# Kernel tuning notes

Measured on AMD Instinct MI355X. Metric: run time of the kernel, lower is better.

Reference implementation:

```python
import jax, jax.numpy as jnp
import numpy as np

B, N, D = 16, 8192, 64
M, S = 256, 32          # npoints, nsample
OUT = 128
RADIUS = 0.4
WC = 64                 # WeightNet output channels
BN_EPS = 1e-5
_BN_SCALE = 1.0 / np.sqrt(1.0 + BN_EPS)  # eval-mode BN, running mean 0 / var 1


def _bn(x, gamma, beta):
    shp = [1] * x.ndim
    shp[1] = -1
    return gamma.reshape(shp) * (x * _BN_SCALE) + beta.reshape(shp)


def _pdist2(a, b):
    # a (B,P,3), b (B,Q,3) -> (B,P,Q) squared distances
    return (jnp.sum(a * a, -1)[:, :, None] + jnp.sum(b * b, -1)[:, None, :]
            - 2.0 * jnp.einsum('bpd,bqd->bpq', a, b))


def _fps(xyz, npoints):
    # furthest point sampling, pointnet2 semantics (start at index 0)
    Bq, Nq, _ = xyz.shape
    first = jnp.zeros((Bq,), jnp.int32)

    def step(carry, _):
        dist, last = carry
        pt = xyz[jnp.arange(Bq), last]                   # (B,3)
        d = jnp.sum((xyz - pt[:, None, :]) ** 2, -1)
        dist = jnp.minimum(dist, d)
        nxt = jnp.argmax(dist, -1).astype(jnp.int32)
        return (dist, nxt), nxt

    init = (jnp.full((Bq, Nq), 1e10, xyz.dtype), first)
    _, rest = jax.lax.scan(step, init, None, length=npoints - 1)
    return jnp.concatenate([first[None], rest], 0).T     # (B, npoints)


def _ball_query(xyz, new_xyz, radius, nsample):
    # first `nsample` indices within radius, pad by repeating first valid index
    d2 = _pdist2(new_xyz, xyz)                           # (B,M,N)
    n = xyz.shape[1]
    key = jnp.where(d2 <= radius * radius, n - jnp.arange(n, dtype=jnp.int32), 0)
    vals, idx = jax.lax.top_k(key, nsample)              # lowest in-radius indices first
    return jnp.where(vals > 0, idx, idx[:, :, :1])


def _group(x_ch, idx):
    # x_ch (B,C,N), idx (B,M,S) -> (B,C,M,S)
    return jax.vmap(lambda f, i: f[:, i])(x_ch, idx)


def setup_inputs():
    key = jax.random.key(0)
    ks = jax.random.split(key, 8)
    f = jnp.float32

    def w(k, o, i):
        return (jax.random.normal(k, (o, i), f) / np.sqrt(i)).astype(f)

    return {
        'xyz': jax.random.uniform(ks[0], (B, N, 3), f),
        'feature': jax.random.normal(ks[1], (B, D, N), f),
        'w0': w(ks[2], WC, 3), 'b0': jnp.zeros((WC,), f), 'gamma0': jnp.ones((WC,), f), 'beta0': jnp.zeros((WC,), f),
        'w1': w(ks[3], WC, WC), 'b1': jnp.zeros((WC,), f), 'gamma1': jnp.ones((WC,), f), 'beta1': jnp.zeros((WC,), f),
        'w2': w(ks[4], WC, WC), 'b2': jnp.zeros((WC,), f),
        'wl': w(ks[5], OUT, D * WC), 'bl': jnp.zeros((OUT,), f), 'gammal': jnp.ones((OUT,), f), 'betal': jnp.zeros((OUT,), f),
        'wf': w(ks[6], OUT, D + OUT), 'bf': jnp.zeros((OUT,), f), 'gammaf': jnp.ones((OUT,), f), 'betaf': jnp.zeros((OUT,), f),
    }


def reference(xyz, feature, w0, b0, gamma0, beta0, w1, b1, gamma1, beta1, w2, b2,
              wl, bl, gammal, betal, wf, bf, gammaf, betaf):
    relu = jax.nn.relu
    # ---- furthest point sampling ----
    fidx = _fps(xyz, M)                                  # (B,M)
    new_xyz = xyz[jnp.arange(B)[:, None], fidx]          # (B,M,3)
    # ---- ball query + grouping ----
    gidx = _ball_query(xyz, new_xyz, RADIUS, S)          # (B,M,S)
    xyz_ch = jnp.transpose(xyz, (0, 2, 1))               # (B,3,N)
    grouped_xyz = _group(xyz_ch, gidx) - jnp.transpose(new_xyz, (0, 2, 1))[:, :, :, None]  # (B,3,M,S) centered
    grouped_feat = _group(feature, gidx)                 # (B,D,M,S)
    # ---- WeightNet (1x1 convs on offsets) ----
    h = relu(_bn(jnp.einsum('oc,bcms->boms', w0, grouped_xyz) + b0[None, :, None, None], gamma0, beta0))
    h = relu(_bn(jnp.einsum('oc,bcms->boms', w1, h) + b1[None, :, None, None], gamma1, beta1))
    weights = jnp.einsum('oc,bcms->boms', w2, h) + b2[None, :, None, None]  # (B,WC,M,S)
    # ---- weighted aggregation: (B,M,D,S) @ (B,M,S,WC) -> (B,M,D*WC) ----
    agg = jnp.einsum('bdms,bwms->bmdw', grouped_feat, weights).reshape(B, M, D * WC)
    new_feature = relu(_bn(jnp.einsum('od,bmd->bom', wl, agg) + bl[None, :, None], gammal, betal))  # (B,OUT,M)
    # ---- three-NN interpolation back to N points ----
    d2 = _pdist2(xyz, new_xyz)                           # (B,N,M)
    negd, nidx = jax.lax.top_k(-d2, 3)                   # 3 nearest sampled centers
    rd = 1.0 / (-negd + 1e-8)                            # reverse density on squared distance
    wts = rd / jnp.sum(rd, -1, keepdims=True)            # (B,N,3)
    gathered = jax.vmap(lambda f2, i: f2[:, i])(new_feature, nidx)  # (B,OUT,N,3)
    interp = jnp.einsum('bcnk,bnk->bcn', gathered, wts)  # (B,OUT,N)
    # ---- concat skip + final 1x1 conv ----
    cat = jnp.concatenate([interp, feature], 1)          # (B,OUT+D,N)
    return relu(_bn(jnp.einsum('oc,bcn->bon', wf, cat) + bf[None, :, None], gammaf, betaf))
```

## Files before the change

kernel.cpp:

```cpp
#include <hip/hip_runtime.h>
#include <hip/hip_bf16.h>
#include <cstdint>
#include <cstddef>

#define BB   16
#define NN   8192
#define DD   64
#define MM   256
#define SS   32
#define OUTC 128
#define WCC  64

using short8 = __attribute__((ext_vector_type(8))) short;
using f32x4  = __attribute__((ext_vector_type(4))) float;

__device__ __forceinline__ float bnf(float x, float g, float be){
    const float BNS = 0.99999500003749969f;
    return g * (x * BNS) + be;
}
__device__ __forceinline__ unsigned short f2bf(float f){
    __hip_bfloat16 h = __float2bfloat16(f);
    return *reinterpret_cast<unsigned short*>(&h);
}
__device__ __forceinline__ float bf2f(unsigned short u){
    return __uint_as_float(((unsigned)u) << 16);
}

#define PRE_GRID (16 + 2048 + 512 + 24)

__global__ __launch_bounds__(256, 1) void k_pre(const float* __restrict__ xyz, float* __restrict__ nxyz,
    const float* __restrict__ feature, unsigned short* __restrict__ featB,
    const float* __restrict__ wl, unsigned short* __restrict__ wlB,
    const float* __restrict__ wf, unsigned short* __restrict__ wfB){
  __shared__ union {
    struct {
      float sxyz[NN*3];
      float snew[MM*3];
      unsigned long long skey[2][4];
    } f;
    float tile[64][65];
  } sm;
  const int t = threadIdx.x;
  int blk = blockIdx.x;

  if (blk < 16){
    const int b = blk;
    const float* xb = xyz + (size_t)b*NN*3;
    for (int i = t; i < NN*3; i += 256) sm.f.sxyz[i] = xb[i];
    float px[32], py[32], pz[32], pn[32], dist[32];
#pragma unroll
    for (int i=0;i<32;i++){
      const int id = i*256 + t;
      px[i] = xb[id*3+0]; py[i] = xb[id*3+1]; pz[i] = xb[id*3+2];
      pn[i] = px[i]*px[i] + py[i]*py[i] + pz[i]*pz[i];
      dist[i] = 1e10f;
    }
    __syncthreads();
    float lx = sm.f.sxyz[0], ly = sm.f.sxyz[1], lz = sm.f.sxyz[2];
    if (t==0){ sm.f.snew[0]=lx; sm.f.snew[1]=ly; sm.f.snew[2]=lz; }
    for (int step=1; step<MM; ++step){
      const float nlx = -2.0f*lx, nly = -2.0f*ly, nlz = -2.0f*lz;
      const float l2s = lx*lx + ly*ly + lz*lz;
      float bv = 0.0f; int bil = 0;
#pragma unroll
      for (int i=0;i<32;i++){
        float c  = pn[i] + l2s;
        float d  = __builtin_fmaf(px[i], nlx, __builtin_fmaf(py[i], nly, __builtin_fmaf(pz[i], nlz, c)));
        float nd = fminf(dist[i], d);
        dist[i] = nd;
        bool gt = nd > bv;
        bv  = gt ? nd : bv;
        bil = gt ? i  : bil;
      }
      const int bi = bil*256 + t;
      float v = bv; int s_;
      s_ = __builtin_amdgcn_update_dpp(__float_as_int(v), __float_as_int(v), 0x111, 0xF, 0xF, 0); v = fmaxf(v, __int_as_float(s_));
      s_ = __builtin_amdgcn_update_dpp(__float_as_int(v), __float_as_int(v), 0x112, 0xF, 0xF, 0); v = fmaxf(v, __int_as_float(s_));
      s_ = __builtin_amdgcn_update_dpp(__float_as_int(v), __float_as_int(v), 0x114, 0xF, 0xF, 0); v = fmaxf(v, __int_as_float(s_));
      s_ = __builtin_amdgcn_update_dpp(__float_as_int(v), __float_as_int(v), 0x118, 0xF, 0xF, 0); v = fmaxf(v, __int_as_float(s_));
      s_ = __builtin_amdgcn_update_dpp(__float_as_int(v), __float_as_int(v), 0x142, 0xF, 0xF, 0); v = fmaxf(v, __int_as_float(s_));
      s_ = __builtin_amdgcn_update_dpp(__float_as_int(v), __float_as_int(v), 0x143, 0xF, 0xF, 0); v = fmaxf(v, __int_as_float(s_));
      const float wmax = __int_as_float(__builtin_amdgcn_readlane(__float_as_int(v), 63));
      unsigned cm = (bv == wmax) ? (unsigned)bi : 0xFFFFFFFFu;
      unsigned u_;
      u_ = (unsigned)__builtin_amdgcn_update_dpp((int)cm, (int)cm, 0x111, 0xF, 0xF, 0); cm = cm < u_ ? cm : u_;
      u_ = (unsigned)__builtin_amdgcn_update_dpp((int)cm, (int)cm, 0x112, 0xF, 0xF, 0); cm = cm < u_ ? cm : u_;
      u_ = (unsigned)__builtin_amdgcn_update_dpp((int)cm, (int)cm, 0x114, 0xF, 0xF, 0); cm = cm < u_ ? cm : u_;
      u_ = (unsigned)__builtin_amdgcn_update_dpp((int)cm, (int)cm, 0x118, 0xF, 0xF, 0); cm = cm < u_ ? cm : u_;
      u_ = (unsigned)__builtin_amdgcn_update_dpp((int)cm, (int)cm, 0x142, 0xF, 0xF, 0); cm = cm < u_ ? cm : u_;
      u_ = (unsigned)__builtin_amdgcn_update_dpp((int)cm, (int)cm, 0x143, 0xF, 0xF, 0); cm = cm < u_ ? cm : u_;
      const unsigned widx = (unsigned)__builtin_amdgcn_readlane((int)cm, 63);
      const unsigned long long key = ((unsigned long long)__float_as_uint(wmax) << 32) | (unsigned)(NN-1 - widx);

      const int p = step & 1;
      if ((t & 63) == 0) sm.f.skey[p][t>>6] = key;
      __syncthreads();
      unsigned long long k0=sm.f.skey[p][0], k1=sm.f.skey[p][1], k2=sm.f.skey[p][2], k3=sm.f.skey[p][3];
      unsigned long long ka = k0>k1?k0:k1, kb = k2>k3?k2:k3;
      unsigned long long kw = ka>kb?ka:kb;
      const int bid = (NN-1) - (int)(unsigned)(kw & 0xFFFFFFFFull);
      lx = sm.f.sxyz[bid*3+0]; ly = sm.f.sxyz[bid*3+1]; lz = sm.f.sxyz[bid*3+2];
      if (t==0){ sm.f.snew[step*3+0]=lx; sm.f.snew[step*3+1]=ly; sm.f.snew[step*3+2]=lz; }
    }
    __syncthreads();
    for (int i = t; i < MM*3; i += 256) nxyz[(size_t)b*MM*3 + i] = sm.f.snew[i];
    return;
  }
  blk -= 16;
  if (blk < 2048){
    const int b  = blk >> 7;
    const int n0 = (blk & 127) << 6;
    {
      const int d = t >> 2, j0 = (t & 3) << 4;
      const float* src = feature + ((size_t)b*DD + d)*NN + n0 + j0;
#pragma unroll
      for (int i=0;i<16;i+=4){
        float4 v = *(const float4*)(src + i);
        sm.tile[d][j0+i+0]=v.x; sm.tile[d][j0+i+1]=v.y; sm.tile[d][j0+i+2]=v.z; sm.tile[d][j0+i+3]=v.w;
      }
    }
    __syncthreads();
    {
      const int j = t >> 2, d0 = (t & 3) << 4;
      unsigned short hv[16];
#pragma unroll
      for (int i=0;i<16;i++) hv[i] = f2bf(sm.tile[d0+i][j]);
      unsigned short* dst = featB + ((size_t)b*NN + n0 + j)*64 + d0;
      *(uint4*)(dst)     = *(uint4*)(&hv[0]);
      *(uint4*)(dst + 8) = *(uint4*)(&hv[8]);
    }
    return;
  }
  blk -= 2048;
  if (blk < 512){
    int idx = (blk*256 + t)*4;
    float4 v = *(const float4*)(wl + idx);
    ushort4 h = make_ushort4(f2bf(v.x), f2bf(v.y), f2bf(v.z), f2bf(v.w));
    *(ushort4*)(wlB + idx) = h;
    return;
  }
  blk -= 512;
  {
    int idx = (blk*256 + t)*4;
    if (idx < 128*192){
      float4 v = *(const float4*)(wf + idx);
      ushort4 h = make_ushort4(f2bf(v.x), f2bf(v.y), f2bf(v.z), f2bf(v.w));
      *(ushort4*)(wfB + idx) = h;
    }
  }
}

__global__ __launch_bounds__(64) void k_bq_mlp(const float* __restrict__ xyz,
    const float* __restrict__ nxyz,
    const float* __restrict__ w0, const float* __restrict__ b0,
    const float* __restrict__ g0, const float* __restrict__ be0,
    const float* __restrict__ w1, const float* __restrict__ b1,
    const float* __restrict__ g1, const float* __restrict__ be1,
    const float* __restrict__ w2, const float* __restrict__ b2,
    int* __restrict__ gidx, float* __restrict__ wbuf){
  const int bm = blockIdx.x;
  const int b  = bm >> 8;
  const int c  = threadIdx.x;
  __shared__ int   sidx[SS];
  __shared__ float sgx[3][SS];
  __shared__ float sh0[SS][WCC];
  __shared__ float sh1[SS][WCC];

  const float w0r0 = w0[c*3+0], w0r1 = w0[c*3+1], w0r2 = w0[c*3+2];
  const float b0c=b0[c], g0c=g0[c], be0c=be0[c];
  const float b1c=b1[c], g1c=g1[c], be1c=be1[c], b2c=b2[c];
  float w1r[64], w2r[64];
#pragma unroll
  for (int i=0;i<16;i++){
    float4 v = *(const float4*)(w1 + c*64 + i*4);
    w1r[i*4+0]=v.x; w1r[i*4+1]=v.y; w1r[i*4+2]=v.z; w1r[i*4+3]=v.w;
    float4 u = *(const float4*)(w2 + c*64 + i*4);
    w2r[i*4+0]=u.x; w2r[i*4+1]=u.y; w2r[i*4+2]=u.z; w2r[i*4+3]=u.w;
  }
  const float cx = nxyz[bm*3+0], cy = nxyz[bm*3+1], cz = nxyz[bm*3+2];
  const float* xb = xyz + (size_t)b*NN*3;
  const float R2 = (float)(0.4*0.4);
  int cnt = 0;
  for (int n0=0; n0<NN && cnt<SS; n0+=64){
    int n = n0 + c;
    float dx = xb[n*3+0]-cx, dy = xb[n*3+1]-cy, dz = xb[n*3+2]-cz;
    float d2 = dx*dx+dy*dy+dz*dz;
    bool in = (d2 <= R2);
    unsigned long long mk = __ballot(in);
    int rank = cnt + (int)__popcll(mk & ((1ull<<c)-1ull));
    if (in && rank < SS) sidx[rank] = n;
    cnt += (int)__popcll(mk);
  }
  int total = min(cnt, SS);
  __syncthreads();
  int i0 = sidx[0];
  if (c >= total && c < SS) sidx[c] = i0;
  __syncthreads();
  if (c < SS){
    int p = sidx[c];
    gidx[bm*SS + c] = p;
    sgx[0][c] = xb[p*3+0]-cx;
    sgx[1][c] = xb[p*3+1]-cy;
    sgx[2][c] = xb[p*3+2]-cz;
  }
  __syncthreads();
  for (int s=0;s<SS;s++){
    float pre = w0r0*sgx[0][s] + w0r1*sgx[1][s] + w0r2*sgx[2][s] + b0c;
    sh0[s][c] = fmaxf(bnf(pre, g0c, be0c), 0.f);
  }
  __syncthreads();
  for (int s=0;s<SS;s++){
    float a = b1c;
#pragma unroll
    for (int k=0;k<64;k+=4){
      float4 h = *(const float4*)(&sh0[s][k]);
      a += w1r[k]*h.x + w1r[k+1]*h.y + w1r[k+2]*h.z + w1r[k+3]*h.w;
    }
    sh1[s][c] = fmaxf(bnf(a, g1c, be1c), 0.f);
  }
  __syncthreads();
  float* wb = wbuf + (size_t)bm*SS*WCC;
  for (int s=0;s<SS;s++){
    float a = b2c;
#pragma unroll
    for (int k=0;k<64;k+=4){
      float4 h = *(const float4*)(&sh1[s][k]);
      a += w2r[k]*h.x + w2r[k+1]*h.y + w2r[k+2]*h.z + w2r[k+3]*h.w;
    }
    wb[s*WCC + c] = a;
  }
}

__global__ __launch_bounds__(256) void k_agg(const unsigned short* __restrict__ featB,
                                             const float* __restrict__ wbuf,
                                             const int* __restrict__ gidx,
                                             unsigned short* __restrict__ aggB){
  const int bm = blockIdx.x;
  const int b  = bm >> 8;
  __shared__ float wt[SS][WCC];
  __shared__ int   sidx[SS];
  const int t = threadIdx.x;
  const float* wsrc = wbuf + (size_t)bm*SS*WCC;
#pragma unroll
  for (int i=0;i<8;i++){
    int li = t + i*256;
    ((float*)wt)[li] = wsrc[li];
  }
  if (t < SS) sidx[t] = gidx[bm*SS + t];
  __syncthreads();
  const int d  = t & 63;
  const int wg = t >> 6;
  float acc[16];
#pragma unroll
  for (int j=0;j<16;j++) acc[j]=0.f;
  const unsigned short* fb = featB + (size_t)b*NN*64;
  for (int s=0;s<SS;s++){
    float fv = bf2f(fb[(size_t)sidx[s]*64 + d]);
#pragma unroll
    for (int j=0;j<16;j++) acc[j] += fv * wt[s][wg*16+j];
  }
  unsigned short h[16];
#pragma unroll
  for (int j=0;j<16;j++) h[j] = f2bf(acc[j]);
  unsigned short* ab = aggB + (size_t)bm*4096 + d*64 + wg*16;
  *(uint4*)(ab)     = *(uint4*)(&h[0]);
  *(uint4*)(ab + 8) = *(uint4*)(&h[8]);
}

__global__ __launch_bounds__(256) void k_nf_part(const unsigned short* __restrict__ aggB,
                                                 const unsigned short* __restrict__ wlB,
                                                 float* __restrict__ part){
  const int blk = blockIdx.x;
  const int rb  = blk >> 2;
  const int ks  = blk & 3;
  const int wid = threadIdx.x >> 6, lane = threadIdx.x & 63;
  const int m0 = rb*64 + wid*16;
  const int r  = lane & 15, kg = lane >> 4;
  f32x4 acc[8];
#pragma unroll
  for (int i=0;i<8;i++) acc[i] = (f32x4){0.f,0.f,0.f,0.f};
  const short* arow = (const short*)aggB + (size_t)(m0 + r)*4096 + ks*1024 + kg*8;
  const short* brow = (const short*)wlB  + (size_t)r*4096        + ks*1024 + kg*8;
#pragma unroll 4
  for (int kc=0; kc<32; kc++){
    short8 a = *(const short8*)(arow + kc*32);
#pragma unroll
    for (int ot=0; ot<8; ot++){
      short8 bfr = *(const short8*)(brow + (size_t)ot*16*4096 + kc*32);
      acc[ot] = __builtin_amdgcn_mfma_f32_16x16x32_bf16(a, bfr, acc[ot], 0, 0, 0);
    }
  }
  float* pb = part + ((size_t)ks << 19);
#pragma unroll
  for (int ot=0; ot<8; ot++){
#pragma unroll
    for (int rr=0; rr<4; rr++){
      int row = m0 + kg*4 + rr;
      pb[(size_t)row*128 + ot*16 + r] = acc[ot][rr];
    }
  }
}

__global__ __launch_bounds__(256) void k_nf_ep(const float* __restrict__ part,
    const float* __restrict__ bl, const float* __restrict__ gl, const float* __restrict__ bel,
    float* __restrict__ nfT){
  const int gid = blockIdx.x*256 + threadIdx.x;
  const int base = gid*4;
  const int o0 = base & 127;
  float4 s0 = *(const float4*)(part + base);
  float4 s1 = *(const float4*)(part + (1<<19) + base);
  float4 s2 = *(const float4*)(part + (2<<19) + base);
  float4 s3 = *(const float4*)(part + (3<<19) + base);
  float sum[4] = {s0.x+s1.x+s2.x+s3.x, s0.y+s1.y+s2.y+s3.y,
                  s0.z+s1.z+s2.z+s3.z, s0.w+s1.w+s2.w+s3.w};
  float ov[4];
#pragma unroll
  for (int j=0;j<4;j++){
    const int o = o0 + j;
    ov[j] = fmaxf(bnf(sum[j] + bl[o], gl[o], bel[o]), 0.f);
  }
  *(float4*)(nfT + base) = make_float4(ov[0],ov[1],ov[2],ov[3]);
}

__global__ __launch_bounds__(256) void k_final(const float* __restrict__ xyz,
    const float* __restrict__ nxyz, const float* __restrict__ nfT,
    const unsigned short* __restrict__ featB, const unsigned short* __restrict__ wfB,
    const float* __restrict__ bf, const float* __restrict__ gf, const float* __restrict__ bef,
    float* __restrict__ out){
  const int blk = blockIdx.x;
  const int b  = blk >> 6;
  const int n0 = (blk & 63) << 7;
  __shared__ float snew[MM*3];
  __shared__ float sw[128][3];
  __shared__ int   si[128][3];
  const int t = threadIdx.x;
  if (t < 192){
    float4 v = *(const float4*)(nxyz + (size_t)b*MM*3 + t*4);
    snew[t*4+0]=v.x; snew[t*4+1]=v.y; snew[t*4+2]=v.z; snew[t*4+3]=v.w;
  }
  __syncthreads();
  if (t < 128){
    const int n = n0 + t;
    const float x = xyz[((size_t)b*NN+n)*3+0];
    const float y = xyz[((size_t)b*NN+n)*3+1];
    const float z = xyz[((size_t)b*NN+n)*3+2];
    float d1=1e30f, d2=1e30f, d3=1e30f; int i1=0,i2=0,i3=0;
    for (int m=0;m<MM;m++){
      float dx=x-snew[m*3+0], dy=y-snew[m*3+1], dz=z-snew[m*3+2];
      float d = dx*dx+dy*dy+dz*dz;
      if (d < d3){
        if (d < d1){ d3=d2;i3=i2; d2=d1;i2=i1; d1=d;i1=m; }
        else if (d < d2){ d3=d2;i3=i2; d2=d;i2=m; }
        else { d3=d;i3=m; }
      }
    }
    float r1=1.f/(d1+1e-8f), r2=1.f/(d2+1e-8f), r3=1.f/(d3+1e-8f);
    float rs = 1.f/(r1+r2+r3);
    sw[t][0]=r1*rs; sw[t][1]=r2*rs; sw[t][2]=r3*rs;
    si[t][0]=i1; si[t][1]=i2; si[t][2]=i3;
  }
  __syncthreads();

  const int w = t >> 6, lane = t & 63;
  const int r = lane & 15, kg = lane >> 4;
  float wA[8][3]; int iA[8][3];
#pragma unroll
  for (int nt=0;nt<8;nt++){
    int n = nt*16 + r;
    wA[nt][0]=sw[n][0]; wA[nt][1]=sw[n][1]; wA[nt][2]=sw[n][2];
    iA[nt][0]=si[n][0]*128; iA[nt][1]=si[n][1]*128; iA[nt][2]=si[n][2]*128;
  }
  const float* nfb = nfT + (size_t)b*MM*128;
  const unsigned short* fbB = featB + ((size_t)b*NN + n0)*64;
  const unsigned short* wfRow0 = wfB + (size_t)(w*32 +      r)*192 + kg*8;
  const unsigned short* wfRow1 = wfB + (size_t)(w*32 + 16 + r)*192 + kg*8;
  f32x4 acc[2][8];
#pragma unroll
  for (int i=0;i<2;i++)
#pragma unroll
    for (int j=0;j<8;j++) acc[i][j] = (f32x4){0.f,0.f,0.f,0.f};

#pragma unroll
  for (int c=0;c<6;c++){
    short8 a0 = *(const short8*)(wfRow0 + c*32);
    short8 a1 = *(const short8*)(wfRow1 + c*32);
    if (c < 4){
      const int k8 = c*32 + kg*8;
#pragma unroll
      for (int nt=0;nt<8;nt++){
        const float* p0 = nfb + iA[nt][0] + k8;
        const float* p1 = nfb + iA[nt][1] + k8;
        const float* p2 = nfb + iA[nt][2] + k8;
        float4 xa = *(const float4*)(p0), xb4 = *(const float4*)(p0+4);
        float4 ya = *(const float4*)(p1), yb4 = *(const float4*)(p1+4);
        float4 za = *(const float4*)(p2), zb4 = *(const float4*)(p2+4);
        const float w0v=wA[nt][0], w1v=wA[nt][1], w2v=wA[nt][2];
        float e0 = w0v*xa.x + w1v*ya.x + w2v*za.x;
        float e1 = w0v*xa.y + w1v*ya.y + w2v*za.y;
        float e2 = w0v*xa.z + w1v*ya.z + w2v*za.z;
        float e3 = w0v*xa.w + w1v*ya.w + w2v*za.w;
        float e4 = w0v*xb4.x + w1v*yb4.x + w2v*zb4.x;
        float e5 = w0v*xb4.y + w1v*yb4.y + w2v*zb4.y;
        float e6 = w0v*xb4.z + w1v*yb4.z + w2v*zb4.z;
        float e7 = w0v*xb4.w + w1v*yb4.w + w2v*zb4.w;
        short8 bfr = { (short)f2bf(e0), (short)f2bf(e1), (short)f2bf(e2), (short)f2bf(e3),
                       (short)f2bf(e4), (short)f2bf(e5), (short)f2bf(e6), (short)f2bf(e7) };
        acc[0][nt] = __builtin_amdgcn_mfma_f32_16x16x32_bf16(a0, bfr, acc[0][nt], 0, 0, 0);
        acc[1][nt] = __builtin_amdgcn_mfma_f32_16x16x32_bf16(a1, bfr, acc[1][nt], 0, 0, 0);
      }
    } else {
      const int d8 = (c-4)*32 + kg*8;
#pragma unroll
      for (int nt=0;nt<8;nt++){
        short8 bfr = *(const short8*)(fbB + (size_t)(nt*16 + r)*64 + d8);
        acc[0][nt] = __builtin_amdgcn_mfma_f32_16x16x32_bf16(a0, bfr, acc[0][nt], 0, 0, 0);
        acc[1][nt] = __builtin_amdgcn_mfma_f32_16x16x32_bf16(a1, bfr, acc[1][nt], 0, 0, 0);
      }
    }
  }
#pragma unroll
  for (int ot=0; ot<2; ot++){
#pragma unroll
    for (int rr=0; rr<4; rr++){
      const int o = w*32 + ot*16 + kg*4 + rr;
      const float bfo = bf[o], gfo = gf[o], befo = bef[o];
      float* dst = out + ((size_t)b*OUTC + o)*NN + n0 + r;
#pragma unroll
      for (int nt=0;nt<8;nt++){
        float val = fmaxf(bnf(acc[ot][nt][rr] + bfo, gfo, befo), 0.f);
        dst[nt*16] = val;
      }
    }
  }
}

extern "C" void kernel_launch(void* const* d_in, const int* in_sizes, int n_in,
                              void* d_out, int out_size, void* d_ws, size_t ws_size,
                              hipStream_t stream){
  const float* xyz     = (const float*)d_in[0];
  const float* feature = (const float*)d_in[1];
  const float* w0  = (const float*)d_in[2];
  const float* b0  = (const float*)d_in[3];
  const float* g0  = (const float*)d_in[4];
  const float* be0 = (const float*)d_in[5];
  const float* w1  = (const float*)d_in[6];
  const float* b1  = (const float*)d_in[7];
  const float* g1  = (const float*)d_in[8];
  const float* be1 = (const float*)d_in[9];
  const float* w2  = (const float*)d_in[10];
  const float* b2  = (const float*)d_in[11];
  const float* wl  = (const float*)d_in[12];
  const float* bl  = (const float*)d_in[13];
  const float* gl  = (const float*)d_in[14];
  const float* bel = (const float*)d_in[15];
  const float* wf  = (const float*)d_in[16];
  const float* bf  = (const float*)d_in[17];
  const float* gf  = (const float*)d_in[18];
  const float* bef = (const float*)d_in[19];
  float* out = (float*)d_out;

  char* ws = (char*)d_ws;
  unsigned short* featB = (unsigned short*)(ws + 0);
  float*          wbuf  = (float*)(ws + 16777216);
  float*          part  = (float*)(ws + 16777216);
  unsigned short* aggB  = (unsigned short*)(ws + 50331648);
  unsigned short* wlB   = (unsigned short*)(ws + 83886080);
  unsigned short* wfB   = (unsigned short*)(ws + 84934656);
  float*          nxyz  = (float*)(ws + 84983808);
  int*            gidx  = (int*)  (ws + 85032960);
  float*          nfT   = (float*)(ws + 85557248);

  k_pre    <<<PRE_GRID, 256, 0, stream>>>(xyz, nxyz, feature, featB, wl, wlB, wf, wfB);
  k_bq_mlp <<<BB*MM, 64, 0, stream>>>(xyz, nxyz, w0,b0,g0,be0, w1,b1,g1,be1, w2,b2, gidx, wbuf);
  k_agg    <<<BB*MM, 256, 0, stream>>>(featB, wbuf, gidx, aggB);
  k_nf_part<<<256,  256, 0, stream>>>(aggB, wlB, part);
  k_nf_ep  <<<512,  256, 0, stream>>>(part, bl, gl, bel, nfT);
  k_final  <<<BB*(NN/128), 256, 0, stream>>>(xyz, nxyz, nfT, featB, wfB, bf, gf, bef, out);
}
```

Before: 575.9 us.

## Fuse split-K GEMM with BN epilogue and pack FPS argmax into one u64 reduction

The split-K partial GEMM kernel and its separate reduce/BN/ReLU epilogue kernel become one kernel that runs the full K loop per block and applies bias, BN and ReLU directly. This removes a kernel launch and the round trip through the partial-sum buffer, but drops the grid from 256 to 64 blocks, so each block runs a four-times-longer K loop with less parallelism. Separately, the FPS wavefront argmax now reduces a packed 64-bit (value, inverted index) key with DPP in one pass instead of a max pass followed by a min-index pass. This shortens the serial per-step chain in the latency-bound FPS loop, at the cost of two DPP moves per stage.

```diff
diff --git a/kernel.cpp b/kernel.cpp
--- a/kernel.cpp
+++ b/kernel.cpp
@@ -73,25 +73,26 @@
         bil = gt ? i  : bil;
       }
       const int bi = bil*256 + t;
-      float v = bv; int s_;
-      s_ = __builtin_amdgcn_update_dpp(__float_as_int(v), __float_as_int(v), 0x111, 0xF, 0xF, 0); v = fmaxf(v, __int_as_float(s_));
-      s_ = __builtin_amdgcn_update_dpp(__float_as_int(v), __float_as_int(v), 0x112, 0xF, 0xF, 0); v = fmaxf(v, __int_as_float(s_));
-      s_ = __builtin_amdgcn_update_dpp(__float_as_int(v), __float_as_int(v), 0x114, 0xF, 0xF, 0); v = fmaxf(v, __int_as_float(s_));
-      s_ = __builtin_amdgcn_update_dpp(__float_as_int(v), __float_as_int(v), 0x118, 0xF, 0xF, 0); v = fmaxf(v, __int_as_float(s_));
-      s_ = __builtin_amdgcn_update_dpp(__float_as_int(v), __float_as_int(v), 0x142, 0xF, 0xF, 0); v = fmaxf(v, __int_as_float(s_));
-      s_ = __builtin_amdgcn_update_dpp(__float_as_int(v), __float_as_int(v), 0x143, 0xF, 0xF, 0); v = fmaxf(v, __int_as_float(s_));
-      const float wmax = __int_as_float(__builtin_amdgcn_readlane(__float_as_int(v), 63));
-      unsigned cm = (bv == wmax) ? (unsigned)bi : 0xFFFFFFFFu;
-      unsigned u_;
-      u_ = (unsigned)__builtin_amdgcn_update_dpp((int)cm, (int)cm, 0x111, 0xF, 0xF, 0); cm = cm < u_ ? cm : u_;
-      u_ = (unsigned)__builtin_amdgcn_update_dpp((int)cm, (int)cm, 0x112, 0xF, 0xF, 0); cm = cm < u_ ? cm : u_;
-      u_ = (unsigned)__builtin_amdgcn_update_dpp((int)cm, (int)cm, 0x114, 0xF, 0xF, 0); cm = cm < u_ ? cm : u_;
-      u_ = (unsigned)__builtin_amdgcn_update_dpp((int)cm, (int)cm, 0x118, 0xF, 0xF, 0); cm = cm < u_ ? cm : u_;
-      u_ = (unsigned)__builtin_amdgcn_update_dpp((int)cm, (int)cm, 0x142, 0xF, 0xF, 0); cm = cm < u_ ? cm : u_;
-      u_ = (unsigned)__builtin_amdgcn_update_dpp((int)cm, (int)cm, 0x143, 0xF, 0xF, 0); cm = cm < u_ ? cm : u_;
-      const unsigned widx = (unsigned)__builtin_amdgcn_readlane((int)cm, 63);
-      const unsigned long long key = ((unsigned long long)__float_as_uint(wmax) << 32) | (unsigned)(NN-1 - widx);
-
+      unsigned long long key = ((unsigned long long)__float_as_uint(bv) << 32) | (unsigned)(NN-1 - bi);
+#define DPP_U64_MAX(CTRL) do { \
+        unsigned lo_ = (unsigned)key, hi_ = (unsigned)(key >> 32); \
+        unsigned olo_ = (unsigned)__builtin_amdgcn_update_dpp((int)lo_, (int)lo_, (CTRL), 0xF, 0xF, 0); \
+        unsigned ohi_ = (unsigned)__builtin_amdgcn_update_dpp((int)hi_, (int)hi_, (CTRL), 0xF, 0xF, 0); \
+        unsigned long long ok_ = ((unsigned long long)ohi_ << 32) | olo_; \
+        key = ok_ > key ? ok_ : key; \
+      } while(0)
+      DPP_U64_MAX(0x111);
+      DPP_U64_MAX(0x112);
+      DPP_U64_MAX(0x114);
+      DPP_U64_MAX(0x118);
+      DPP_U64_MAX(0x142);
+      DPP_U64_MAX(0x143);
+#undef DPP_U64_MAX
+      {
+        unsigned klo = (unsigned)__builtin_amdgcn_readlane((int)(unsigned)key, 63);
+        unsigned khi = (unsigned)__builtin_amdgcn_readlane((int)(unsigned)(key >> 32), 63);
+        key = ((unsigned long long)khi << 32) | klo;
+      }
       const int p = step & 1;
       if ((t & 63) == 0) sm.f.skey[p][t>>6] = key;
       __syncthreads();
@@ -267,22 +268,21 @@
   *(uint4*)(ab + 8) = *(uint4*)(&h[8]);
 }
 
-__global__ __launch_bounds__(256) void k_nf_part(const unsigned short* __restrict__ aggB,
-                                                 const unsigned short* __restrict__ wlB,
-                                                 float* __restrict__ part){
-  const int blk = blockIdx.x;
-  const int rb  = blk >> 2;
-  const int ks  = blk & 3;
+__global__ __launch_bounds__(256) void k_nf(const unsigned short* __restrict__ aggB,
+                                            const unsigned short* __restrict__ wlB,
+    const float* __restrict__ bl, const float* __restrict__ gl, const float* __restrict__ bel,
+    float* __restrict__ nfT){
+  const int rb  = blockIdx.x;
   const int wid = threadIdx.x >> 6, lane = threadIdx.x & 63;
   const int m0 = rb*64 + wid*16;
   const int r  = lane & 15, kg = lane >> 4;
   f32x4 acc[8];
 #pragma unroll
   for (int i=0;i<8;i++) acc[i] = (f32x4){0.f,0.f,0.f,0.f};
-  const short* arow = (const short*)aggB + (size_t)(m0 + r)*4096 + ks*1024 + kg*8;
-  const short* brow = (const short*)wlB  + (size_t)r*4096        + ks*1024 + kg*8;
+  const short* arow = (const short*)aggB + (size_t)(m0 + r)*4096 + kg*8;
+  const short* brow = (const short*)wlB  + (size_t)r*4096        + kg*8;
 #pragma unroll 4
-  for (int kc=0; kc<32; kc++){
+  for (int kc=0; kc<128; kc++){
     short8 a = *(const short8*)(arow + kc*32);
 #pragma unroll
     for (int ot=0; ot<8; ot++){
@@ -290,36 +290,15 @@
       acc[ot] = __builtin_amdgcn_mfma_f32_16x16x32_bf16(a, bfr, acc[ot], 0, 0, 0);
     }
   }
-  float* pb = part + ((size_t)ks << 19);
 #pragma unroll
   for (int ot=0; ot<8; ot++){
 #pragma unroll
     for (int rr=0; rr<4; rr++){
-      int row = m0 + kg*4 + rr;
-      pb[(size_t)row*128 + ot*16 + r] = acc[ot][rr];
-    }
-  }
-}
-
-__global__ __launch_bounds__(256) void k_nf_ep(const float* __restrict__ part,
-    const float* __restrict__ bl, const float* __restrict__ gl, const float* __restrict__ bel,
-    float* __restrict__ nfT){
-  const int gid = blockIdx.x*256 + threadIdx.x;
-  const int base = gid*4;
-  const int o0 = base & 127;
-  float4 s0 = *(const float4*)(part + base);
-  float4 s1 = *(const float4*)(part + (1<<19) + base);
-  float4 s2 = *(const float4*)(part + (2<<19) + base);
-  float4 s3 = *(const float4*)(part + (3<<19) + base);
-  float sum[4] = {s0.x+s1.x+s2.x+s3.x, s0.y+s1.y+s2.y+s3.y,
-                  s0.z+s1.z+s2.z+s3.z, s0.w+s1.w+s2.w+s3.w};
-  float ov[4];
-#pragma unroll
-  for (int j=0;j<4;j++){
-    const int o = o0 + j;
-    ov[j] = fmaxf(bnf(sum[j] + bl[o], gl[o], bel[o]), 0.f);
-  }
-  *(float4*)(nfT + base) = make_float4(ov[0],ov[1],ov[2],ov[3]);
+      const int row = m0 + kg*4 + rr;
+      const int o   = ot*16 + r;
+      nfT[(size_t)row*128 + o] = fmaxf(bnf(acc[ot][rr] + bl[o], gl[o], bel[o]), 0.f);
+    }
+  }
 }
 
 __global__ __launch_bounds__(256) void k_final(const float* __restrict__ xyz,
@@ -462,7 +441,6 @@
   char* ws = (char*)d_ws;
   unsigned short* featB = (unsigned short*)(ws + 0);
   float*          wbuf  = (float*)(ws + 16777216);
-  float*          part  = (float*)(ws + 16777216);
   unsigned short* aggB  = (unsigned short*)(ws + 50331648);
   unsigned short* wlB   = (unsigned short*)(ws + 83886080);
   unsigned short* wfB   = (unsigned short*)(ws + 84934656);
@@ -473,7 +451,6 @@
   k_pre    <<<PRE_GRID, 256, 0, stream>>>(xyz, nxyz, feature, featB, wl, wlB, wf, wfB);
   k_bq_mlp <<<BB*MM, 64, 0, stream>>>(xyz, nxyz, w0,b0,g0,be0, w1,b1,g1,be1, w2,b2, gidx, wbuf);
   k_agg    <<<BB*MM, 256, 0, stream>>>(featB, wbuf, gidx, aggB);
-  k_nf_part<<<256,  256, 0, stream>>>(aggB, wlB, part);
-  k_nf_ep  <<<512,  256, 0, stream>>>(part, bl, gl, bel, nfT);
+  k_nf     <<<64,   256, 0, stream>>>(aggB, wlB, bl, gl, bel, nfT);
   k_final  <<<BB*(NN/128), 256, 0, stream>>>(xyz, nxyz, nfT, featB, wfB, bf, gf, bef, out);
 }
```

Result: slower. 741.5 us (+28.7%).
